# Kernel tuning notes

Measured on AMD Instinct MI355X. Metric: run time of the kernel, lower is better.

Reference implementation:

```python
import jax, jax.numpy as jnp
import numpy as np

NUM_HEADS = 16

def setup_inputs() -> dict:
    key = jax.random.key(0)
    k1, k2, k3 = jax.random.split(key, 3)
    B, T, D = 4, 2048, 1024
    x = jax.random.normal(k1, (B, T, D), dtype=jnp.float32)
    # lecun_normal: std = 1/sqrt(fan_in)
    w = jax.random.normal(k2, (3 * D, D), dtype=jnp.float32) * (1.0 / np.sqrt(D))
    w_out = jax.random.normal(k3, (D, D), dtype=jnp.float32) * (1.0 / np.sqrt(D))
    return {"x": x, "w": w, "w_out": w_out}


def reference(x, w, w_out):
    B, T, D = x.shape
    H = NUM_HEADS
    L = D // H
    # qkv projection: (B,T,3D)
    q, k, v = jnp.split(jnp.matmul(x, w.T), 3, axis=2)
    # -> (T,B,H,L) time-major for the scan
    q = q.reshape(B, T, H, L).transpose(1, 0, 2, 3)
    k = k.reshape(B, T, H, L).transpose(1, 0, 2, 3)
    v = v.reshape(B, T, H, L).transpose(1, 0, 2, 3)
    scale = jax.lax.rsqrt(jnp.float32(L))
    k_exp = jnp.exp(k * scale) + 1e-6            # (T,B,H,L)
    k_norm = jnp.cumsum(k_exp, axis=0)           # causal normalizer
    qs = jax.nn.softmax(q * scale, axis=-1) / k_norm

    def step(carry, args):
        qs_t, k_t, v_t = args                    # each (B,H,L)
        # accumulate outer product k_t v_t^T into (B,H,L,L) state
        carry = carry + k_t[..., :, None] * v_t[..., None, :]
        y_t = jnp.einsum('bhl,bhlm->bhm', qs_t, carry)
        return carry, y_t

    init = jnp.zeros((B, H, L, L), dtype=x.dtype)
    _, y = jax.lax.scan(step, init, (qs, k_exp, v))   # y: (T,B,H,L)
    y = y.reshape(T, B, D).transpose(1, 0, 2)         # (B,T,D)
    return jnp.matmul(y, w_out)                       # Dense, no bias
```

## Files before the change

### kernel.cpp

```cpp
#include <hip/hip_runtime.h>
#include <math.h>

#define Bsz   4
#define Tsz   2048
#define Dsz   1024
#define Hsz   16
#define Lsz   64
#define BHsz  64
#define CH    64
#define NCH   32
#define QKVLD 3072
#define SCL   0.125f
#define QSC   512.0f
#define QSCI  (1.0f/512.0f)

typedef float  floatx4 __attribute__((ext_vector_type(4)));
typedef _Float16 half8 __attribute__((ext_vector_type(8)));
typedef _Float16 half4v __attribute__((ext_vector_type(4)));
typedef _Float16 half2v __attribute__((ext_vector_type(2)));

#define AS1 __attribute__((address_space(1)))
#define AS3 __attribute__((address_space(3)))

static __device__ __forceinline__ void gload_lds16(const void* g, void* l) {
  __builtin_amdgcn_global_load_lds((const AS1 unsigned int*)g,
                                   (AS3 unsigned int*)l, 16, 0, 0);
}

static __device__ __forceinline__ float wave_sum64(float v) {
#pragma unroll
  for (int off = 1; off < 64; off <<= 1) v += __shfl_xor(v, off);
  return v;
}

__launch_bounds__(256)
__global__ void prep(const float* __restrict__ x, _Float16* __restrict__ xh,
                     const float* __restrict__ w, _Float16* __restrict__ wh,
                     const float* __restrict__ wo, _Float16* __restrict__ woT) {
  const int blk = blockIdx.x, tid = threadIdx.x;
  if (blk < 11264) {
    const float* in  = (blk < 8192) ? x : w;
    _Float16*   outp = (blk < 8192) ? xh : wh;
    const int bi = (blk < 8192) ? blk : blk - 8192;
    const int i = (bi * 256 + tid) * 4;
    float4 v = *(const float4*)(in + i);
    half4v h = { (_Float16)v.x, (_Float16)v.y, (_Float16)v.z, (_Float16)v.w };
    *(half4v*)(outp + i) = h;
  } else {
    __shared__ float tile[32][33];
    const int bi = blk - 11264;
    const int bx = (bi & 31) * 32;
    const int by = (bi >> 5) * 32;
    const int tx = tid & 31, ty0 = tid >> 5;
#pragma unroll
    for (int p = 0; p < 4; p++) {
      const int ty = ty0 + p * 8;
      tile[ty][tx] = wo[(size_t)(by + ty) * 1024 + bx + tx];
    }
    __syncthreads();
#pragma unroll
    for (int p = 0; p < 4; p++) {
      const int ty = ty0 + p * 8;
      woT[(size_t)(bx + ty) * 1024 + by + tx] = (_Float16)tile[tx][ty];
    }
  }
}

__launch_bounds__(512, 2)
__global__ void qkv_gemm8(const _Float16* __restrict__ A, const _Float16* __restrict__ B,
                          _Float16* __restrict__ C) {
  __shared__ __align__(16) _Float16 AsF[2 * 256 * 64];
  __shared__ __align__(16) _Float16 BsF[2 * 256 * 64];
  const int tid  = threadIdx.x;
  const int wv   = tid >> 6, lane = tid & 63;
  const int wm   = wv >> 2, wn = wv & 3;
  const int fr   = lane & 15, fq = lane >> 4;

  const int flat = blockIdx.x;
  const int g  = (flat & 7) * 48 + (flat >> 3);
  const int m0 = (g / 12) * 256;
  const int n0 = (g % 12) * 256;

  const int srow = lane >> 3;
  const int scg  = (lane & 7) ^ srow;
  const int wv8  = wv * 8;
  const _Float16* aSrc = A + (size_t)(m0 + wv8 + srow) * 1024 + scg * 8;
  const _Float16* bSrc = B + (size_t)(n0 + wv8 + srow) * 1024 + scg * 8;

  const int sw  = fr & 7;
  const int ck0 = ((0 + fq) ^ sw) * 8;
  const int ck1 = ((4 + fq) ^ sw) * 8;
  const _Float16* apt = AsF + (wm * 64 + fr) * 64;
  const _Float16* bpt = BsF + (wn * 32 + fr) * 64;

  floatx4 acc[8][4];
#pragma unroll
  for (int i = 0; i < 8; i++)
#pragma unroll
    for (int j = 0; j < 4; j++) acc[i][j] = (floatx4){0.f, 0.f, 0.f, 0.f};

  half8 aF[8];
  half8 bF0[4], bF1[4];

#define BAR2() do { __builtin_amdgcn_s_barrier();                              \
                    asm volatile("" ::: "memory"); } while (0)
#define VMW4() asm volatile("s_waitcnt vmcnt(4)" ::: "memory")
#define SYNC() do { __builtin_amdgcn_s_barrier();                              \
    asm volatile("s_waitcnt lgkmcnt(0)" ::: "memory");                         \
    __builtin_amdgcn_sched_barrier(0); } while (0)

#define STAGE_A(kt, hm, sbuf) do {                                             \
    const _Float16* s_ = aSrc + (hm) * (128 * 1024) + (kt) * 64;               \
    gload_lds16(s_,             &AsF[(sbuf) * 16384 + ((hm) * 128 + wv8) * 64]);      \
    gload_lds16(s_ + 64 * 1024, &AsF[(sbuf) * 16384 + ((hm) * 128 + 64 + wv8) * 64]); \
  } while (0)
#define STAGE_B(kt, hm, sbuf) do {                                             \
    const _Float16* s_ = bSrc + (hm) * (128 * 1024) + (kt) * 64;               \
    gload_lds16(s_,             &BsF[(sbuf) * 16384 + ((hm) * 128 + wv8) * 64]);      \
    gload_lds16(s_ + 64 * 1024, &BsF[(sbuf) * 16384 + ((hm) * 128 + 64 + wv8) * 64]); \
  } while (0)

#define RD_A(buf, qm) do {                                                     \
    _Pragma("unroll")                                                          \
    for (int mf = 0; mf < 4; mf++) {                                           \
      const _Float16* p_ = apt + (buf) * 16384 + (qm) * 8192 + mf * 1024;      \
      aF[mf * 2]     = *(const half8*)(p_ + ck0);                              \
      aF[mf * 2 + 1] = *(const half8*)(p_ + ck1);                              \
    } } while (0)
#define RD_B(buf, qn, dst) do {                                                \
    _Pragma("unroll")                                                          \
    for (int nf = 0; nf < 2; nf++) {                                           \
      const _Float16* p_ = bpt + (buf) * 16384 + (qn) * 8192 + nf * 1024;      \
      dst[nf * 2]     = *(const half8*)(p_ + ck0);                             \
      dst[nf * 2 + 1] = *(const half8*)(p_ + ck1);                             \
    } } while (0)

#define MM(qm, qn, bb) do {                                                    \
    __builtin_amdgcn_s_setprio(1);                                             \
    _Pragma("unroll")                                                          \
    for (int mf = 0; mf < 4; mf++)                                             \
      _Pragma("unroll")                                                        \
      for (int nf = 0; nf < 2; nf++) {                                         \
        acc[(qm) * 4 + mf][(qn) * 2 + nf] = __builtin_amdgcn_mfma_f32_16x16x32_f16( \
            aF[mf * 2], bb[nf * 2], acc[(qm) * 4 + mf][(qn) * 2 + nf], 0, 0, 0);     \
        acc[(qm) * 4 + mf][(qn) * 2 + nf] = __builtin_amdgcn_mfma_f32_16x16x32_f16( \
            aF[mf * 2 + 1], bb[nf * 2 + 1], acc[(qm) * 4 + mf][(qn) * 2 + nf], 0, 0, 0); \
      }                                                                        \
    __builtin_amdgcn_s_setprio(0);                                             \
  } while (0)

  STAGE_A(0, 0, 0); STAGE_B(0, 0, 0); STAGE_A(0, 1, 0); STAGE_B(0, 1, 0);
  STAGE_A(1, 0, 1); STAGE_B(1, 0, 1);
  VMW4(); BAR2();

#pragma unroll 1
  for (int t = 0; t < 16; t += 2) {
    RD_A(0, 0); RD_B(0, 0, bF0); STAGE_A(t + 1, 1, 1);
    SYNC(); MM(0, 0, bF0); BAR2();

    RD_B(0, 1, bF1); STAGE_B(t + 1, 1, 1); STAGE_A(t + 2, 0, 0);
    SYNC(); MM(0, 1, bF1); BAR2();

    RD_A(0, 1); STAGE_B(t + 2, 0, 0);
    SYNC(); MM(1, 1, bF1); BAR2();

    VMW4();
    SYNC(); MM(1, 0, bF0); BAR2();

    RD_A(1, 0); RD_B(1, 0, bF0); STAGE_A(t + 2, 1, 0);
    SYNC(); MM(0, 0, bF0); BAR2();

    RD_B(1, 1, bF1); STAGE_B(t + 2, 1, 0); STAGE_A(t + 3, 0, 1);
    SYNC(); MM(0, 1, bF1); BAR2();

    RD_A(1, 1); STAGE_B(t + 3, 0, 1);
    SYNC(); MM(1, 1, bF1); BAR2();

    VMW4();
    SYNC(); MM(1, 0, bF0); BAR2();
  }

#undef MM
#undef RD_B
#undef RD_A
#undef STAGE_B
#undef STAGE_A
#undef SYNC
#undef VMW4
#undef BAR2

  const bool kreg = (n0 >= 1024) && (n0 < 2048);
#pragma unroll
  for (int qm = 0; qm < 2; qm++)
#pragma unroll
    for (int mf = 0; mf < 4; mf++) {
      const int row = m0 + qm * 128 + wm * 64 + mf * 16 + fq * 4;
#pragma unroll
      for (int qn = 0; qn < 2; qn++)
#pragma unroll
        for (int nf = 0; nf < 2; nf++) {
          const int col = n0 + qn * 128 + wn * 32 + nf * 16 + fr;
#pragma unroll
          for (int r = 0; r < 4; r++) {
            float v = acc[qm * 4 + mf][qn * 2 + nf][r];
            if (kreg) v = __expf(v * SCL) + 1e-6f;
            C[(size_t)(row + r) * 3072 + col] = (_Float16)v;
          }
        }
    }
}

__launch_bounds__(256)
__global__ void gemm2(const _Float16* __restrict__ A, const _Float16* __restrict__ B,
                      float* __restrict__ C) {
  __shared__ __align__(16) _Float16 As[2][128][32];
  __shared__ __align__(16) _Float16 Bs[2][128][32];
  const int tid = threadIdx.x;
  const int wv = tid >> 6, lane = tid & 63;
  const int wm = wv >> 1, wn = wv & 1;
  const int fr = lane & 15, fq = lane >> 4;

  const int flat = blockIdx.x;
  const int xcd = flat & 7, loc = flat >> 3;
  const int m0 = (xcd * 8 + (loc >> 3)) * 128;
  const int n0 = (loc & 7) * 128;

  const int srow = lane >> 2;
  const int scg  = lane & 3;
  const _Float16* aSrc = A + (size_t)(m0 + wv * 32 + srow) * 1024 + scg * 8;
  const _Float16* bSrc = B + (size_t)(n0 + wv * 32 + srow) * 1024 + scg * 8;
  _Float16* aBase = &As[0][0][0];
  _Float16* bBase = &Bs[0][0][0];

  const _Float16* apt = aBase + (wm * 64 + fr) * 32 + fq * 8;
  const _Float16* bpt = bBase + (wn * 64 + fr) * 32 + fq * 8;

  floatx4 acc[4][4];
#pragma unroll
  for (int i = 0; i < 4; i++)
#pragma unroll
    for (int j = 0; j < 4; j++) acc[i][j] = (floatx4){0.f, 0.f, 0.f, 0.f};

  half8 aF[4], bF[4];

#define BAR2() do { __builtin_amdgcn_s_barrier();                              \
                    asm volatile("" ::: "memory"); } while (0)
#define VMW4() asm volatile("s_waitcnt vmcnt(4)" ::: "memory")
#define SYNC() do { __builtin_amdgcn_s_barrier();                              \
    asm volatile("s_waitcnt lgkmcnt(0)" ::: "memory");                         \
    __builtin_amdgcn_sched_barrier(0); } while (0)

#define STAGE(kt, bufi) do {                                                   \
    const _Float16* sa_ = aSrc + (size_t)(kt) * 32;                            \
    const _Float16* sb_ = bSrc + (size_t)(kt) * 32;                            \
    gload_lds16(sa_,             aBase + (bufi) * 4096 + (wv * 32) * 32 + lane * 8);      \
    gload_lds16(sa_ + 16 * 1024, aBase + (bufi) * 4096 + (wv * 32 + 16) * 32 + lane * 8); \
    gload_lds16(sb_,             bBase + (bufi) * 4096 + (wv * 32) * 32 + lane * 8);      \
    gload_lds16(sb_ + 16 * 1024, bBase + (bufi) * 4096 + (wv * 32 + 16) * 32 + lane * 8); \
  } while (0)

#define RD8(bufi) do {                                                         \
    _Pragma("unroll")                                                          \
    for (int mf = 0; mf < 4; mf++)                                             \
      aF[mf] = *(const half8*)(apt + (bufi) * 4096 + mf * 512);                \
    _Pragma("unroll")                                                          \
    for (int nf = 0; nf < 4; nf++)                                             \
      bF[nf] = *(const half8*)(bpt + (bufi) * 4096 + nf * 512);                \
  } while (0)

#define MM16() do {                                                            \
    __builtin_amdgcn_s_setprio(1);                                             \
    _Pragma("unroll")                                                          \
    for (int mt = 0; mt < 4; mt++)                                             \
      _Pragma("unroll")                                                        \
      for (int nt = 0; nt < 4; nt++)                                           \
        acc[mt][nt] = __builtin_amdgcn_mfma_f32_16x16x32_f16(aF[mt], bF[nt],   \
                                                             acc[mt][nt], 0, 0, 0); \
    __builtin_amdgcn_s_setprio(0);                                             \
  } while (0)

  STAGE(0, 0);
  STAGE(1, 1);
  VMW4(); BAR2();

#pragma unroll 1
  for (int t = 0; t < 32; t += 2) {
    RD8(0);
    SYNC(); MM16(); BAR2();
    STAGE(t + 2, 0);
    VMW4();
    BAR2();

    RD8(1);
    SYNC(); MM16(); BAR2();
    STAGE(t + 3, 1);
    VMW4();
    BAR2();
  }

#undef MM16
#undef RD8
#undef STAGE
#undef SYNC
#undef VMW4
#undef BAR2

#pragma unroll
  for (int mt = 0; mt < 4; mt++) {
    const int row = m0 + wm * 64 + mt * 16 + fq * 4;
#pragma unroll
    for (int nt = 0; nt < 4; nt++) {
      const int col = n0 + wn * 64 + nt * 16 + fr;
#pragma unroll
      for (int r = 0; r < 4; r++)
        C[(size_t)(row + r) * 1024 + col] = acc[mt][nt][r];
    }
  }
}

__launch_bounds__(256)
__global__ void chunk_kv(const _Float16* __restrict__ qkv, _Float16* __restrict__ KV,
                         float* __restrict__ Ksum) {
  const int blk = blockIdx.x;
  const int bh = blk >> 5, c = blk & 31;
  const int b = bh >> 4, h = bh & 15;
  const int tid = threadIdx.x;
  const int wave = tid >> 6, lane = tid & 63;
  const int fr = lane & 15, fq = lane >> 4;
  const int m2  = (tid & 31) * 2;
  const int tg8 = (tid >> 5) * 8;

  __shared__ __align__(16) _Float16 KxT[64][72];
  __shared__ __align__(16) _Float16 VT [64][72];

  const size_t base = ((size_t)(b * Tsz + c * CH)) * QKVLD + h * 64;
  half8 klo, khi, vlo, vhi;
#pragma unroll
  for (int j = 0; j < 8; j++) {
    const int t = tg8 + j;
    half2v kk = *(const half2v*)(qkv + base + (size_t)t * QKVLD + 1024 + m2);
    klo[j] = kk[0]; khi[j] = kk[1];
    half2v vv = *(const half2v*)(qkv + base + (size_t)t * QKVLD + 2048 + m2);
    vlo[j] = vv[0]; vhi[j] = vv[1];
  }
  *(half8*)&KxT[m2][tg8]     = klo;
  *(half8*)&KxT[m2 + 1][tg8] = khi;
  *(half8*)&VT[m2][tg8]      = vlo;
  *(half8*)&VT[m2 + 1][tg8]  = vhi;
  __syncthreads();

  floatx4 acc[4];
#pragma unroll
  for (int j = 0; j < 4; j++) acc[j] = (floatx4){0.f, 0.f, 0.f, 0.f};
#pragma unroll
  for (int ks = 0; ks < 2; ks++) {
    half8 av = *(const half8*)&VT[wave * 16 + fr][ks * 32 + fq * 8];
#pragma unroll
    for (int j = 0; j < 4; j++) {
      half8 bv = *(const half8*)&KxT[j * 16 + fr][ks * 32 + fq * 8];
      acc[j] = __builtin_amdgcn_mfma_f32_16x16x32_f16(av, bv, acc[j], 0, 0, 0);
    }
  }
  _Float16* KVp = KV + ((size_t)(bh * NCH + c)) * 4096;
#pragma unroll
  for (int j = 0; j < 4; j++)
#pragma unroll
    for (int r = 0; r < 4; r++)
      KVp[(wave * 16 + fq * 4 + r) * 64 + j * 16 + fr] = (_Float16)acc[j][r];

  if (tid < 64) {
    float s = 0.f;
    const half8* row = (const half8*)&KxT[tid][0];
#pragma unroll
    for (int j8 = 0; j8 < 8; j8++) {
      half8 v8 = row[j8];
#pragma unroll
      for (int j = 0; j < 8; j++) s += (float)v8[j];
    }
    Ksum[(bh * NCH + c) * 64 + tid] = s;
  }
}

__launch_bounds__(256)
__global__ void prefix_kern(_Float16* __restrict__ KV, float* __restrict__ Ksum) {
  const int cid = blockIdx.x * 256 + threadIdx.x;
  const int bh = cid >> 11, e2 = cid & 2047;
  half2v* p = (half2v*)(KV + (size_t)bh * NCH * 4096) + e2;
  float ax = 0.f, ay = 0.f;
#pragma unroll
  for (int c = 0; c < NCH; c++) {
    half2v t = p[(size_t)c * 2048];
    half2v o = { (_Float16)ax, (_Float16)ay };
    p[(size_t)c * 2048] = o;
    ax += (float)t[0]; ay += (float)t[1];
  }
  if (cid < 1024) {
    const int kbh = cid >> 4, l4 = cid & 15;
    float4* kp = (float4*)(Ksum + (size_t)kbh * NCH * 64) + l4;
    float4 acc = {0.f, 0.f, 0.f, 0.f};
#pragma unroll
    for (int c = 0; c < NCH; c++) {
      float4 t = kp[c * 16];
      kp[c * 16] = acc;
      acc.x += t.x; acc.y += t.y; acc.z += t.z; acc.w += t.w;
    }
  }
}

__launch_bounds__(256)
__global__ void chunk_y(const _Float16* __restrict__ qkv, const _Float16* __restrict__ KV,
                        const float* __restrict__ Ksum, _Float16* __restrict__ Y) {
  const int bh = blockIdx.x, c = blockIdx.y;
  const int b = bh >> 4, h = bh & 15;
  const int tid = threadIdx.x;
  const int wave = tid >> 6, lane = tid & 63;
  const int fr = lane & 15, fq = lane >> 4;

  __shared__ __align__(16) _Float16 kxh[64][72];
  __shared__ __align__(16) _Float16 kxT[64][72];
  __shared__ __align__(16) _Float16 Ph[64][136];
  __shared__ __align__(16) _Float16 Bh[64][136];

  const size_t base = ((size_t)(b * Tsz + c * CH)) * QKVLD + h * 64;
  const _Float16* KVp = KV + ((size_t)(bh * NCH + c)) * 4096;
  const int ksoff = (bh * NCH + c) * 64;

  _Float16 qreg[16];
#pragma unroll
  for (int i = 0; i < 16; i++)
    qreg[i] = qkv[base + (size_t)(wave * 16 + i) * QKVLD + lane];

  float ksb[4];
#pragma unroll
  for (int j = 0; j < 4; j++) ksb[j] = Ksum[ksoff + j * 16 + fr];

  {
    const int rr  = tid >> 3;
    const int sg8 = (tid & 7) * 8;
#pragma unroll
    for (int p = 0; p < 2; p++) {
      const int t = p * 32 + rr;
      *(half8*)&kxh[t][sg8] =
          *(const half8*)(qkv + base + (size_t)t * QKVLD + 1024 + sg8);
      *(half8*)&Ph[t][64 + sg8] =
          *(const half8*)(qkv + base + (size_t)t * QKVLD + 2048 + sg8);
    }
  }
  {
    const int m  = tid >> 2;
    const int l0 = (tid & 3) * 16;
    *(half8*)&Bh[m][l0]     = *(const half8*)(KVp + m * 64 + l0);
    *(half8*)&Bh[m][l0 + 8] = *(const half8*)(KVp + m * 64 + l0 + 8);
  }
  __syncthreads();

  {
    const int l2  = (tid & 31) * 2;
    const int tg8 = (tid >> 5) * 8;
    half8 k0, k1, v0, v1;
#pragma unroll
    for (int j = 0; j < 8; j++) {
      const int t = tg8 + j;
      half2v kk = *(const half2v*)&kxh[t][l2];
      k0[j] = kk[0]; k1[j] = kk[1];
      half2v vv = *(const half2v*)&Ph[t][64 + l2];
      v0[j] = vv[0]; v1[j] = vv[1];
    }
    *(half8*)&kxT[l2][tg8]          = k0;
    *(half8*)&kxT[l2 + 1][tg8]      = k1;
    *(half8*)&Bh[l2][64 + tg8]      = v0;
    *(half8*)&Bh[l2 + 1][64 + tg8]  = v1;
  }
  __syncthreads();

  {
    floatx4 kacc[4];
#pragma unroll
    for (int j = 0; j < 4; j++) kacc[j] = (floatx4){0.f, 0.f, 0.f, 0.f};
#pragma unroll
    for (int ks = 0; ks < 2; ks++) {
      half8 af;
#pragma unroll
      for (int j = 0; j < 8; j++)
        af[j] = (ks * 32 + fq * 8 + j) <= (wave * 16 + fr) ? (_Float16)1.0f
                                                           : (_Float16)0.0f;
#pragma unroll
      for (int j = 0; j < 4; j++) {
        half8 bf = *(const half8*)&kxT[j * 16 + fr][ks * 32 + fq * 8];
        kacc[j] = __builtin_amdgcn_mfma_f32_16x16x32_f16(af, bf, kacc[j], 0, 0, 0);
      }
    }
    __syncthreads();
#pragma unroll
    for (int j = 0; j < 4; j++)
#pragma unroll
      for (int r = 0; r < 4; r++)
        kxT[wave * 16 + fq * 4 + r][j * 16 + fr] =
            (_Float16)(QSC / (ksb[j] + kacc[j][r]));
  }

#pragma unroll
  for (int i = 0; i < 16; i++) {
    const int t = wave * 16 + i;
    float e = __expf((float)qreg[i] * SCL);
    float s = wave_sum64(e);
    Ph[t][lane] = (_Float16)((e / s) * (float)kxT[t][lane]);
  }
  __syncthreads();

  const int wm = (wave >> 1) * 32, wn = (wave & 1) * 32;
  {
    floatx4 a2[2][2];
#pragma unroll
    for (int mt = 0; mt < 2; mt++)
#pragma unroll
      for (int nt = 0; nt < 2; nt++) a2[mt][nt] = (floatx4){0.f, 0.f, 0.f, 0.f};
#pragma unroll
    for (int ks = 0; ks < 2; ks++) {
      half8 af[2], bf[2];
#pragma unroll
      for (int i = 0; i < 2; i++) {
        af[i] = *(const half8*)&Ph[wm + i * 16 + fr][ks * 32 + fq * 8];
        bf[i] = *(const half8*)&kxh[wn + i * 16 + fr][ks * 32 + fq * 8];
      }
#pragma unroll
      for (int mt = 0; mt < 2; mt++)
#pragma unroll
        for (int nt = 0; nt < 2; nt++)
          a2[mt][nt] = __builtin_amdgcn_mfma_f32_16x16x32_f16(af[mt], bf[nt], a2[mt][nt], 0, 0, 0);
    }
#pragma unroll
    for (int mt = 0; mt < 2; mt++)
#pragma unroll
      for (int nt = 0; nt < 2; nt++)
#pragma unroll
        for (int r = 0; r < 4; r++) {
          const int t = wm + mt * 16 + fq * 4 + r;
          const int s = wn + nt * 16 + fr;
          Ph[t][64 + s] = (_Float16)(s <= t ? a2[mt][nt][r] : 0.f);
        }
  }
  __syncthreads();

  {
    floatx4 acc[2][2];
#pragma unroll
    for (int mt = 0; mt < 2; mt++)
#pragma unroll
      for (int nt = 0; nt < 2; nt++) acc[mt][nt] = (floatx4){0.f, 0.f, 0.f, 0.f};
#pragma unroll
    for (int ks = 0; ks < 4; ks++) {
      half8 af[2], bf[2];
#pragma unroll
      for (int i = 0; i < 2; i++) {
        af[i] = *(const half8*)&Ph[wm + i * 16 + fr][ks * 32 + fq * 8];
        bf[i] = *(const half8*)&Bh[wn + i * 16 + fr][ks * 32 + fq * 8];
      }
#pragma unroll
      for (int mt = 0; mt < 2; mt++)
#pragma unroll
        for (int nt = 0; nt < 2; nt++)
          acc[mt][nt] = __builtin_amdgcn_mfma_f32_16x16x32_f16(af[mt], bf[nt], acc[mt][nt], 0, 0, 0);
    }
#pragma unroll
    for (int mt = 0; mt < 2; mt++)
#pragma unroll
      for (int nt = 0; nt < 2; nt++)
#pragma unroll
        for (int r = 0; r < 4; r++)
          kxh[wm + mt * 16 + fq * 4 + r][wn + nt * 16 + fr] =
              (_Float16)(acc[mt][nt][r] * QSCI);
  }
  __syncthreads();

  {
    const int ty = tid >> 2, sg = (tid & 3) * 16;
    _Float16* yrow = Y + (size_t)(b * Tsz + c * CH + ty) * Dsz + h * 64 + sg;
    *(half8*)(yrow)     = *(const half8*)&kxh[ty][sg];
    *(half8*)(yrow + 8) = *(const half8*)&kxh[ty][sg + 8];
  }
}

extern "C" void kernel_launch(void* const* d_in, const int* in_sizes, int n_in,
                              void* d_out, int out_size, void* d_ws, size_t ws_size,
                              hipStream_t stream) {
  const float* x     = (const float*)d_in[0];
  const float* w     = (const float*)d_in[1];
  const float* w_out = (const float*)d_in[2];
  float* out = (float*)d_out;

  _Float16* xh   = (_Float16*)d_ws;
  _Float16* Yh   = xh;
  _Float16* wh   = xh + (size_t)8192 * 1024;
  _Float16* woT  = wh + (size_t)3072 * 1024;
  _Float16* qkvh = woT + (size_t)1024 * 1024;
  _Float16* KV   = qkvh + (size_t)8192 * 3072;
  float* Ksum = (float*)(KV + (size_t)BHsz * NCH * 4096);

  prep<<<12288, 256, 0, stream>>>(x, xh, w, wh, w_out, woT);

  qkv_gemm8<<<384, 512, 0, stream>>>(xh, wh, qkvh);

  chunk_kv<<<2048, 256, 0, stream>>>(qkvh, KV, Ksum);
  prefix_kern<<<512, 256, 0, stream>>>(KV, Ksum);
  chunk_y<<<dim3(BHsz, NCH), 256, 0, stream>>>(qkvh, KV, Ksum, Yh);

  gemm2<<<512, 256, 0, stream>>>(Yh, woT, out);
}
```

Baseline: 230.7 us.

## Replace 256x256 eight-wave QKV GEMM with simpler 128x128 four-wave tiled kernel

Swaps the QKV projection GEMM from a 256x256-tile, 512-thread kernel with a swizzled LDS layout and an interleaved quarter-tile schedule for a 128x128-tile, 256-thread kernel. The new kernel uses K-steps of 32 with double buffering and no LDS swizzle, modelled on the existing output GEMM. It launches four times as many blocks with a plain stage/compute loop. Smaller tiles lower per-block data reuse and the unswizzled LDS reads may hit bank conflicts, while the simpler schedule may improve occupancy or tail behaviour.

Measured after the change: 234.2 us. No clear change (+1.5%).

```diff
diff --git a/kernel.cpp b/kernel.cpp
--- a/kernel.cpp
+++ b/kernel.cpp
@@ -66,41 +66,38 @@
   }
 }
 
-__launch_bounds__(512, 2)
-__global__ void qkv_gemm8(const _Float16* __restrict__ A, const _Float16* __restrict__ B,
-                          _Float16* __restrict__ C) {
-  __shared__ __align__(16) _Float16 AsF[2 * 256 * 64];
-  __shared__ __align__(16) _Float16 BsF[2 * 256 * 64];
-  const int tid  = threadIdx.x;
-  const int wv   = tid >> 6, lane = tid & 63;
-  const int wm   = wv >> 2, wn = wv & 3;
-  const int fr   = lane & 15, fq = lane >> 4;
+__launch_bounds__(256)
+__global__ void qkv_gemm(const _Float16* __restrict__ A, const _Float16* __restrict__ B,
+                         _Float16* __restrict__ C) {
+  __shared__ __align__(16) _Float16 As[2][128][32];
+  __shared__ __align__(16) _Float16 Bs[2][128][32];
+  const int tid = threadIdx.x;
+  const int wv = tid >> 6, lane = tid & 63;
+  const int wm = wv >> 1, wn = wv & 1;
+  const int fr = lane & 15, fq = lane >> 4;
 
   const int flat = blockIdx.x;
-  const int g  = (flat & 7) * 48 + (flat >> 3);
-  const int m0 = (g / 12) * 256;
-  const int n0 = (g % 12) * 256;
-
-  const int srow = lane >> 3;
-  const int scg  = (lane & 7) ^ srow;
-  const int wv8  = wv * 8;
-  const _Float16* aSrc = A + (size_t)(m0 + wv8 + srow) * 1024 + scg * 8;
-  const _Float16* bSrc = B + (size_t)(n0 + wv8 + srow) * 1024 + scg * 8;
-
-  const int sw  = fr & 7;
-  const int ck0 = ((0 + fq) ^ sw) * 8;
-  const int ck1 = ((4 + fq) ^ sw) * 8;
-  const _Float16* apt = AsF + (wm * 64 + fr) * 64;
-  const _Float16* bpt = BsF + (wn * 32 + fr) * 64;
-
-  floatx4 acc[8][4];
-#pragma unroll
-  for (int i = 0; i < 8; i++)
+  const int xcd = flat & 7, loc = flat >> 3;
+  const int m0 = (xcd * 8 + loc / 24) * 128;
+  const int n0 = (loc % 24) * 128;
+
+  const int srow = lane >> 2;
+  const int scg  = lane & 3;
+  const _Float16* aSrc = A + (size_t)(m0 + wv * 32 + srow) * 1024 + scg * 8;
+  const _Float16* bSrc = B + (size_t)(n0 + wv * 32 + srow) * 1024 + scg * 8;
+  _Float16* aBase = &As[0][0][0];
+  _Float16* bBase = &Bs[0][0][0];
+
+  const _Float16* apt = aBase + (wm * 64 + fr) * 32 + fq * 8;
+  const _Float16* bpt = bBase + (wn * 64 + fr) * 32 + fq * 8;
+
+  floatx4 acc[4][4];
+#pragma unroll
+  for (int i = 0; i < 4; i++)
 #pragma unroll
     for (int j = 0; j < 4; j++) acc[i][j] = (floatx4){0.f, 0.f, 0.f, 0.f};
 
-  half8 aF[8];
-  half8 bF0[4], bF1[4];
+  half8 aF[4], bF[4];
 
 #define BAR2() do { __builtin_amdgcn_s_barrier();                              \
                     asm volatile("" ::: "memory"); } while (0)
@@ -109,105 +106,76 @@
     asm volatile("s_waitcnt lgkmcnt(0)" ::: "memory");                         \
     __builtin_amdgcn_sched_barrier(0); } while (0)
 
-#define STAGE_A(kt, hm, sbuf) do {                                             \
-    const _Float16* s_ = aSrc + (hm) * (128 * 1024) + (kt) * 64;               \
-    gload_lds16(s_,             &AsF[(sbuf) * 16384 + ((hm) * 128 + wv8) * 64]);      \
-    gload_lds16(s_ + 64 * 1024, &AsF[(sbuf) * 16384 + ((hm) * 128 + 64 + wv8) * 64]); \
+#define STAGE(kt, bufi) do {                                                   \
+    const _Float16* sa_ = aSrc + (size_t)(kt) * 32;                            \
+    const _Float16* sb_ = bSrc + (size_t)(kt) * 32;                            \
+    gload_lds16(sa_,             aBase + (bufi) * 4096 + (wv * 32) * 32 + lane * 8);      \
+    gload_lds16(sa_ + 16 * 1024, aBase + (bufi) * 4096 + (wv * 32 + 16) * 32 + lane * 8); \
+    gload_lds16(sb_,             bBase + (bufi) * 4096 + (wv * 32) * 32 + lane * 8);      \
+    gload_lds16(sb_ + 16 * 1024, bBase + (bufi) * 4096 + (wv * 32 + 16) * 32 + lane * 8); \
   } while (0)
-#define STAGE_B(kt, hm, sbuf) do {                                             \
-    const _Float16* s_ = bSrc + (hm) * (128 * 1024) + (kt) * 64;               \
-    gload_lds16(s_,             &BsF[(sbuf) * 16384 + ((hm) * 128 + wv8) * 64]);      \
-    gload_lds16(s_ + 64 * 1024, &BsF[(sbuf) * 16384 + ((hm) * 128 + 64 + wv8) * 64]); \
+
+#define RD8(bufi) do {                                                         \
+    _Pragma("unroll")                                                          \
+    for (int mf = 0; mf < 4; mf++)                                             \
+      aF[mf] = *(const half8*)(apt + (bufi) * 4096 + mf * 512);                \
+    _Pragma("unroll")                                                          \
+    for (int nf = 0; nf < 4; nf++)                                             \
+      bF[nf] = *(const half8*)(bpt + (bufi) * 4096 + nf * 512);                \
   } while (0)
 
-#define RD_A(buf, qm) do {                                                     \
-    _Pragma("unroll")                                                          \
-    for (int mf = 0; mf < 4; mf++) {                                           \
-      const _Float16* p_ = apt + (buf) * 16384 + (qm) * 8192 + mf * 1024;      \
-      aF[mf * 2]     = *(const half8*)(p_ + ck0);                              \
-      aF[mf * 2 + 1] = *(const half8*)(p_ + ck1);                              \
-    } } while (0)
-#define RD_B(buf, qn, dst) do {                                                \
-    _Pragma("unroll")                                                          \
-    for (int nf = 0; nf < 2; nf++) {                                           \
-      const _Float16* p_ = bpt + (buf) * 16384 + (qn) * 8192 + nf * 1024;      \
-      dst[nf * 2]     = *(const half8*)(p_ + ck0);                             \
-      dst[nf * 2 + 1] = *(const half8*)(p_ + ck1);                             \
-    } } while (0)
-
-#define MM(qm, qn, bb) do {                                                    \
+#define MM16() do {                                                            \
     __builtin_amdgcn_s_setprio(1);                                             \
     _Pragma("unroll")                                                          \
-    for (int mf = 0; mf < 4; mf++)                                             \
+    for (int mt = 0; mt < 4; mt++)                                             \
       _Pragma("unroll")                                                        \
-      for (int nf = 0; nf < 2; nf++) {                                         \
-        acc[(qm) * 4 + mf][(qn) * 2 + nf] = __builtin_amdgcn_mfma_f32_16x16x32_f16( \
-            aF[mf * 2], bb[nf * 2], acc[(qm) * 4 + mf][(qn) * 2 + nf], 0, 0, 0);     \
-        acc[(qm) * 4 + mf][(qn) * 2 + nf] = __builtin_amdgcn_mfma_f32_16x16x32_f16( \
-            aF[mf * 2 + 1], bb[nf * 2 + 1], acc[(qm) * 4 + mf][(qn) * 2 + nf], 0, 0, 0); \
-      }                                                                        \
+      for (int nt = 0; nt < 4; nt++)                                           \
+        acc[mt][nt] = __builtin_amdgcn_mfma_f32_16x16x32_f16(aF[mt], bF[nt],   \
+                                                             acc[mt][nt], 0, 0, 0); \
     __builtin_amdgcn_s_setprio(0);                                             \
   } while (0)
 
-  STAGE_A(0, 0, 0); STAGE_B(0, 0, 0); STAGE_A(0, 1, 0); STAGE_B(0, 1, 0);
-  STAGE_A(1, 0, 1); STAGE_B(1, 0, 1);
+  STAGE(0, 0);
+  STAGE(1, 1);
   VMW4(); BAR2();
 
 #pragma unroll 1
-  for (int t = 0; t < 16; t += 2) {
-    RD_A(0, 0); RD_B(0, 0, bF0); STAGE_A(t + 1, 1, 1);
-    SYNC(); MM(0, 0, bF0); BAR2();
-
-    RD_B(0, 1, bF1); STAGE_B(t + 1, 1, 1); STAGE_A(t + 2, 0, 0);
-    SYNC(); MM(0, 1, bF1); BAR2();
-
-    RD_A(0, 1); STAGE_B(t + 2, 0, 0);
-    SYNC(); MM(1, 1, bF1); BAR2();
-
+  for (int t = 0; t < 32; t += 2) {
+    RD8(0);
+    SYNC(); MM16(); BAR2();
+    STAGE(t + 2, 0);
     VMW4();
-    SYNC(); MM(1, 0, bF0); BAR2();
-
-    RD_A(1, 0); RD_B(1, 0, bF0); STAGE_A(t + 2, 1, 0);
-    SYNC(); MM(0, 0, bF0); BAR2();
-
-    RD_B(1, 1, bF1); STAGE_B(t + 2, 1, 0); STAGE_A(t + 3, 0, 1);
-    SYNC(); MM(0, 1, bF1); BAR2();
-
-    RD_A(1, 1); STAGE_B(t + 3, 0, 1);
-    SYNC(); MM(1, 1, bF1); BAR2();
-
+    BAR2();
+
+    RD8(1);
+    SYNC(); MM16(); BAR2();
+    STAGE(t + 3, 1);
     VMW4();
-    SYNC(); MM(1, 0, bF0); BAR2();
-  }
-
-#undef MM
-#undef RD_B
-#undef RD_A
-#undef STAGE_B
-#undef STAGE_A
+    BAR2();
+  }
+
+#undef MM16
+#undef RD8
+#undef STAGE
 #undef SYNC
 #undef VMW4
 #undef BAR2
 
   const bool kreg = (n0 >= 1024) && (n0 < 2048);
 #pragma unroll
-  for (int qm = 0; qm < 2; qm++)
-#pragma unroll
-    for (int mf = 0; mf < 4; mf++) {
-      const int row = m0 + qm * 128 + wm * 64 + mf * 16 + fq * 4;
-#pragma unroll
-      for (int qn = 0; qn < 2; qn++)
-#pragma unroll
-        for (int nf = 0; nf < 2; nf++) {
-          const int col = n0 + qn * 128 + wn * 32 + nf * 16 + fr;
-#pragma unroll
-          for (int r = 0; r < 4; r++) {
-            float v = acc[qm * 4 + mf][qn * 2 + nf][r];
-            if (kreg) v = __expf(v * SCL) + 1e-6f;
-            C[(size_t)(row + r) * 3072 + col] = (_Float16)v;
-          }
-        }
-    }
+  for (int mt = 0; mt < 4; mt++) {
+    const int row = m0 + wm * 64 + mt * 16 + fq * 4;
+#pragma unroll
+    for (int nt = 0; nt < 4; nt++) {
+      const int col = n0 + wn * 64 + nt * 16 + fr;
+#pragma unroll
+      for (int r = 0; r < 4; r++) {
+        float v = acc[mt][nt][r];
+        if (kreg) v = __expf(v * SCL) + 1e-6f;
+        C[(size_t)(row + r) * 3072 + col] = (_Float16)v;
+      }
+    }
+  }
 }
 
 __launch_bounds__(256)
@@ -599,7 +567,7 @@
 
   prep<<<12288, 256, 0, stream>>>(x, xh, w, wh, w_out, woT);
 
-  qkv_gemm8<<<384, 512, 0, stream>>>(xh, wh, qkvh);
+  qkv_gemm<<<1536, 256, 0, stream>>>(xh, wh, qkvh);
 
   chunk_kv<<<2048, 256, 0, stream>>>(qkvh, KV, Ksum);
   prefix_kern<<<512, 256, 0, stream>>>(KV, Ksum);
```
